# Kernel optimization log

Hardware: AMD Instinct MI355X
Metric: run time of the kernel (lower is better)

Reference implementation:

```python
import jax, jax.numpy as jnp
import numpy as np

BASE_K = 256
MAX_K = 512


def setup_inputs() -> dict:
    key = jax.random.key(0)
    kq, ks, kw, kb = jax.random.split(key, 4)
    B, S, D = 4, 4096, 1024
    Q = jax.random.normal(kq, (B, S, D), dtype=jnp.float32)
    scores = jax.random.normal(ks, (B, S, S), dtype=jnp.float32)
    # importance_net = nn.Linear(dim, 1): weight [1, dim], bias [1]
    bound = 1.0 / np.sqrt(D)
    W = jax.random.uniform(kw, (D,), dtype=jnp.float32, minval=-bound, maxval=bound)
    b = jax.random.uniform(kb, (1,), dtype=jnp.float32, minval=-bound, maxval=bound)
    return {"Q": Q, "scores": scores, "W": W, "b": b}


def reference(Q, scores, W, b):
    # importance gate: sigmoid(Linear(Q)) -> [B, S]
    importance = jax.nn.sigmoid(jnp.einsum("bsd,d->bs", Q, W) + b[0])
    # k per query; torch .long() truncates toward zero (values positive -> floor)
    k_per_query = (BASE_K + (MAX_K - BASE_K) * importance).astype(jnp.int32)
    # torch code does `indices, values = torch.topk(...)`, so the returned
    # 'indices' are actually the top-k VALUES. Reproduce faithfully.
    topk_values, _ = jax.lax.top_k(scores, MAX_K)  # [B, S, MAX_K]
    return topk_values, k_per_query
```

## Files before the change

### kernel.cpp

```cpp
#include <hip/hip_runtime.h>

#define SDIM 4096
#define DDIM 1024
#define NROWS 16384
#define KOUT 512

__device__ __forceinline__ unsigned f2key(float f) {
    unsigned u = __float_as_uint(f);
    return (u & 0x80000000u) ? ~u : (u | 0x80000000u);
}
__device__ __forceinline__ float key2f(unsigned k) {
    unsigned u = (k & 0x80000000u) ? (k ^ 0x80000000u) : ~k;
    return __uint_as_float(u);
}
__device__ __forceinline__ unsigned lt_popc(unsigned long long m) {
    return __builtin_amdgcn_mbcnt_hi((unsigned)(m >> 32),
           __builtin_amdgcn_mbcnt_lo((unsigned)(m & 0xFFFFFFFFull), 0u));
}

__global__ __launch_bounds__(256, 1) void fused_kernel(
    const float* __restrict__ scores, const float* __restrict__ Q,
    const float* __restrict__ W, const float* __restrict__ bias,
    float* __restrict__ out_topk, float* __restrict__ out_k) {

    __shared__ unsigned sel[4][KOUT];

    const int tid  = threadIdx.x;
    const int lane = tid & 63;
    const int wid  = tid >> 6;
    const int row  = blockIdx.x * 4 + wid;

    {
        const float4* q4 = (const float4*)(Q + (size_t)row * DDIM);
        const float4* w4 = (const float4*)W;
        float g = 0.f;
#pragma unroll
        for (int i = 0; i < 4; ++i) {
            float4 a = q4[lane + 64 * i];
            float4 b = w4[lane + 64 * i];
            g += a.x * b.x + a.y * b.y + a.z * b.z + a.w * b.w;
        }
#pragma unroll
        for (int off = 32; off; off >>= 1) g += __shfl_down(g, off, 64);
        if (lane == 0) {
            float x   = g + bias[0];
            float imp = 1.0f / (1.0f + expf(-x));
            out_k[row] = (float)(int)(256.0f + 256.0f * imp);
        }
    }

    unsigned key[64];
    {
        const float4* src = (const float4*)(scores + (size_t)row * SDIM);
#pragma unroll
        for (int i = 0; i < 16; ++i) {
            float4 v = src[lane + 64 * i];
            key[4 * i + 0] = f2key(v.x);
            key[4 * i + 1] = f2key(v.y);
            key[4 * i + 2] = f2key(v.z);
            key[4 * i + 3] = f2key(v.w);
        }
    }

    unsigned prefix = 0;
#pragma unroll 1
    for (int b = 31; b >= 0; --b) {
        const unsigned cand = prefix | (1u << b);
        unsigned total = 0;
#pragma unroll
        for (int i = 0; i < 64; ++i)
            total += (unsigned)__popcll(__ballot(key[i] >= cand));
        if (total >= (unsigned)KOUT) {
            prefix = cand;
            if (total == (unsigned)KOUT) break;
        }
    }
    unsigned tmin = 0xFFFFFFFFu;
#pragma unroll
    for (int i = 0; i < 64; ++i) {
        unsigned t = (key[i] >= prefix) ? key[i] : 0xFFFFFFFFu;
        tmin = t < tmin ? t : tmin;
    }
#pragma unroll
    for (int off = 32; off; off >>= 1) {
        unsigned o = __shfl_xor(tmin, off, 64);
        tmin = o < tmin ? o : tmin;
    }
    const unsigned T = tmin;

    unsigned mtot = 0;
#pragma unroll
    for (int i = 0; i < 64; ++i) {
        bool p = key[i] > T;
        unsigned long long m = __ballot(p);
        if (p) sel[wid][mtot + lt_popc(m)] = key[i];
        mtot += (unsigned)__popcll(m);
    }

    __syncthreads();

    unsigned x[8];
#pragma unroll
    for (int r = 0; r < 8; ++r) {
        unsigned idx = 8 * (unsigned)lane + r;
        unsigned v = sel[wid][idx];
        x[r] = (idx < mtot) ? v : T;
    }

#pragma unroll
    for (int kk = 2; kk <= 512; kk <<= 1) {
#pragma unroll
        for (int j = kk >> 1; j >= 8; j >>= 1) {
            bool km = ((((8 * lane) & kk) == 0) == (((8 * lane) & j) == 0));
#pragma unroll
            for (int r = 0; r < 8; ++r) {
                unsigned p  = __shfl_xor(x[r], j >> 3, 64);
                unsigned mx = x[r] > p ? x[r] : p;
                unsigned mn = x[r] > p ? p : x[r];
                x[r] = km ? mx : mn;
            }
        }
#pragma unroll
        for (int j = (kk >> 1) < 4 ? (kk >> 1) : 4; j >= 1; j >>= 1) {
#pragma unroll
            for (int r = 0; r < 8; ++r) {
                if ((r & j) == 0) {
                    int rp = r | j;
                    unsigned a = x[r], b = x[rp];
                    bool d = (((8 * lane + r) & kk) == 0);
                    unsigned hi = a > b ? a : b;
                    unsigned lo = a > b ? b : a;
                    x[r]  = d ? hi : lo;
                    x[rp] = d ? lo : hi;
                }
            }
        }
    }

    float4* dst = (float4*)(out_topk + (size_t)row * KOUT);
    dst[2 * lane + 0] = make_float4(key2f(x[0]), key2f(x[1]), key2f(x[2]), key2f(x[3]));
    dst[2 * lane + 1] = make_float4(key2f(x[4]), key2f(x[5]), key2f(x[6]), key2f(x[7]));
}

extern "C" void kernel_launch(void* const* d_in, const int* in_sizes, int n_in,
                              void* d_out, int out_size, void* d_ws, size_t ws_size,
                              hipStream_t stream) {
    const float* Q      = (const float*)d_in[0];
    const float* scores = (const float*)d_in[1];
    const float* W      = (const float*)d_in[2];
    const float* b      = (const float*)d_in[3];
    float* out_topk = (float*)d_out;
    float* out_k    = (float*)d_out + (size_t)NROWS * KOUT;

    fused_kernel<<<NROWS / 4, 256, 0, stream>>>(scores, Q, W, b, out_topk, out_k);
}
```

Measured before the change: 497.5 us.

## Compact radix-select candidates into LDS once count drops below 1024

The bit-by-bit radix select now stops scanning all 64 keys per lane once the candidate count falls to 1024 or fewer. Those candidates are compacted into a per-wave LDS buffer and the remaining bits are resolved over 16 registers per lane instead of 64. The block-wide __syncthreads is replaced by a wave-local lgkmcnt wait, since each wave only touches its own LDS slice. This cuts ballot/popcount work for the low bits, at the cost of extra LDS traffic and a larger shared footprint. The else branch (count never drops below 1024) sets T=prefix directly.

```diff
diff --git a/kernel.cpp b/kernel.cpp
--- a/kernel.cpp
+++ b/kernel.cpp
@@ -4,6 +4,7 @@
 #define DDIM 1024
 #define NROWS 16384
 #define KOUT 512
+#define CAP 1024
 
 __device__ __forceinline__ unsigned f2key(float f) {
     unsigned u = __float_as_uint(f);
@@ -16,6 +17,9 @@
 __device__ __forceinline__ unsigned lt_popc(unsigned long long m) {
     return __builtin_amdgcn_mbcnt_hi((unsigned)(m >> 32),
            __builtin_amdgcn_mbcnt_lo((unsigned)(m & 0xFFFFFFFFull), 0u));
+}
+__device__ __forceinline__ void wave_lds_fence() {
+    asm volatile("s_waitcnt lgkmcnt(0)" ::: "memory");
 }
 
 __global__ __launch_bounds__(256, 1) void fused_kernel(
@@ -24,6 +28,7 @@
     float* __restrict__ out_topk, float* __restrict__ out_k) {
 
     __shared__ unsigned sel[4][KOUT];
+    __shared__ unsigned cbuf[4][CAP];
 
     const int tid  = threadIdx.x;
     const int lane = tid & 63;
@@ -63,41 +68,94 @@
     }
 
     unsigned prefix = 0;
+    unsigned cnt    = 4096;
+    int      bnext  = -1;
+    bool     trig   = false;
 #pragma unroll 1
     for (int b = 31; b >= 0; --b) {
-        const unsigned cand = prefix | (1u << b);
+        const unsigned candk = prefix | (1u << b);
         unsigned total = 0;
 #pragma unroll
         for (int i = 0; i < 64; ++i)
-            total += (unsigned)__popcll(__ballot(key[i] >= cand));
+            total += (unsigned)__popcll(__ballot(key[i] >= candk));
         if (total >= (unsigned)KOUT) {
-            prefix = cand;
-            if (total == (unsigned)KOUT) break;
-        }
-    }
-    unsigned tmin = 0xFFFFFFFFu;
-#pragma unroll
-    for (int i = 0; i < 64; ++i) {
-        unsigned t = (key[i] >= prefix) ? key[i] : 0xFFFFFFFFu;
-        tmin = t < tmin ? t : tmin;
-    }
-#pragma unroll
-    for (int off = 32; off; off >>= 1) {
-        unsigned o = __shfl_xor(tmin, off, 64);
-        tmin = o < tmin ? o : tmin;
-    }
-    const unsigned T = tmin;
-
+            prefix = candk;
+            cnt    = total;
+            if (cnt <= (unsigned)CAP) { bnext = b - 1; trig = true; break; }
+        }
+    }
+
+    unsigned T;
     unsigned mtot = 0;
-#pragma unroll
-    for (int i = 0; i < 64; ++i) {
-        bool p = key[i] > T;
-        unsigned long long m = __ballot(p);
-        if (p) sel[wid][mtot + lt_popc(m)] = key[i];
-        mtot += (unsigned)__popcll(m);
-    }
-
-    __syncthreads();
+
+    if (trig) {
+        {
+            unsigned c = 0;
+#pragma unroll
+            for (int i = 0; i < 64; ++i) {
+                bool p = key[i] >= prefix;
+                unsigned long long m = __ballot(p);
+                if (p) cbuf[wid][c + lt_popc(m)] = key[i];
+                c += (unsigned)__popcll(m);
+            }
+        }
+        wave_lds_fence();
+
+        unsigned ck[16];
+#pragma unroll
+        for (int j = 0; j < 16; ++j) {
+            unsigned idx = (unsigned)lane + 64u * (unsigned)j;
+            unsigned v = cbuf[wid][idx];
+            ck[j] = (idx < cnt) ? v : 0u;
+        }
+
+        if (cnt > (unsigned)KOUT) {
+#pragma unroll 1
+            for (int b = bnext; b >= 0; --b) {
+                const unsigned candk = prefix | (1u << b);
+                unsigned total = 0;
+#pragma unroll
+                for (int j = 0; j < 16; ++j)
+                    total += (unsigned)__popcll(__ballot(ck[j] >= candk));
+                if (total >= (unsigned)KOUT) {
+                    prefix = candk;
+                    if (total == (unsigned)KOUT) break;
+                }
+            }
+        }
+
+        unsigned tmin = 0xFFFFFFFFu;
+#pragma unroll
+        for (int j = 0; j < 16; ++j) {
+            unsigned t = (ck[j] >= prefix) ? ck[j] : 0xFFFFFFFFu;
+            tmin = t < tmin ? t : tmin;
+        }
+#pragma unroll
+        for (int off = 32; off; off >>= 1) {
+            unsigned o = __shfl_xor(tmin, off, 64);
+            tmin = o < tmin ? o : tmin;
+        }
+        T = tmin;
+
+#pragma unroll
+        for (int j = 0; j < 16; ++j) {
+            bool p = ck[j] > T;
+            unsigned long long m = __ballot(p);
+            if (p) sel[wid][mtot + lt_popc(m)] = ck[j];
+            mtot += (unsigned)__popcll(m);
+        }
+    } else {
+        T = prefix;
+#pragma unroll
+        for (int i = 0; i < 64; ++i) {
+            bool p = key[i] > T;
+            unsigned long long m = __ballot(p);
+            if (p) sel[wid][mtot + lt_popc(m)] = key[i];
+            mtot += (unsigned)__popcll(m);
+        }
+    }
+
+    wave_lds_fence();
 
     unsigned x[8];
 #pragma unroll
```

Result: faster. 457.1 us (-8.1%).
